# Optimization experiments

Hardware: AMD Instinct MI355X
Metric: run time of the kernel (lower is better)

The kernel has to match this reference:

```python
import jax, jax.numpy as jnp
import numpy as np

N_NODES = 50000
N_EDGES = 800000

def _sage_conv(x, src, dst, W, b, n_nodes):
    # DGL SAGEConv aggregator_type='gcn':
    #   h_neigh = (sum_{u in N(v)} x_u + x_v) / (in_deg(v) + 1)
    #   out = h_neigh @ W.T + b   (fc_self unused for gcn aggregator)
    agg = jax.ops.segment_sum(x[src], dst, num_segments=n_nodes)  # [N, d]
    deg = jax.ops.segment_sum(jnp.ones((src.shape[0],), x.dtype), dst, num_segments=n_nodes)
    h = (agg + x) / (deg + 1.0)[:, None]
    return h @ W.T + b

def setup_inputs() -> dict:
    key = jax.random.key(0)
    ks = jax.random.split(key, 9)
    d_in, d_hid, d_out = 128, 128, 64
    x = jax.random.normal(ks[0], (N_NODES, d_in), dtype=jnp.float32)
    src = jax.random.randint(ks[1], (N_EDGES,), 0, N_NODES, dtype=jnp.int32)
    dst = jax.random.randint(ks[2], (N_EDGES,), 0, N_NODES, dtype=jnp.int32)
    def glorot(k, shape):
        fan = shape[0] + shape[1]
        return jax.random.normal(k, shape, dtype=jnp.float32) * jnp.sqrt(2.0 / fan)
    W1 = glorot(ks[3], (d_hid, d_in))
    b1 = jnp.zeros((d_hid,), jnp.float32)
    W2 = glorot(ks[4], (d_hid, d_hid))
    b2 = jnp.zeros((d_hid,), jnp.float32)
    W3 = glorot(ks[5], (d_out, d_hid))
    b3 = jnp.zeros((d_out,), jnp.float32)
    return {"x": x, "src": src, "dst": dst, "W1": W1, "b1": b1,
            "W2": W2, "b2": b2, "W3": W3, "b3": b3}

def reference(x, src, dst, W1, b1, W2, b2, W3, b3):
    n = x.shape[0]
    h = jax.nn.relu(_sage_conv(x, src, dst, W1, b1, n))
    h = jax.nn.relu(_sage_conv(h, src, dst, W2, b2, n))
    h = jax.nn.sigmoid(_sage_conv(h, src, dst, W3, b3, n))
    return h
```

## Files before the change

kernel.cpp:

```cpp
#include <hip/hip_runtime.h>
#include <hip/hip_bf16.h>
#include <math.h>


#define NFEAT 128
#define BSH   7
#define NBUKP 512
#define EPB2  1024
#define CAP   4000

typedef __attribute__((ext_vector_type(8))) short bf16x8;
typedef __attribute__((ext_vector_type(4))) float f32x4;

__device__ __forceinline__ unsigned short f2bf(float f) {
    unsigned u = __float_as_uint(f);
    u += 0x7fffu + ((u >> 16) & 1u);
    return (unsigned short)(u >> 16);
}
__device__ __forceinline__ float bflo(unsigned u) { return __uint_as_float(u << 16); }
__device__ __forceinline__ float bfhi(unsigned u) { return __uint_as_float(u & 0xffff0000u); }


__global__ __launch_bounds__(256) void build_scatter(const int* __restrict__ src,
                                                     const int* __restrict__ dst,
                                                     int* __restrict__ cursor,
                                                     unsigned long long* __restrict__ pairs,
                                                     int E) {
    __shared__ int hist[NBUKP];
    __shared__ int sc[NBUKP];
    __shared__ int lcur[NBUKP];
    __shared__ int lbase[NBUKP];
    __shared__ unsigned long long stage[EPB2];
    __shared__ int destIdx[EPB2];
    __shared__ int nLocalSh;

    const int t = threadIdx.x;
    hist[t] = 0; hist[t + 256] = 0;
    lcur[t] = 0; lcur[t + 256] = 0;
    __syncthreads();

    const int base = blockIdx.x * EPB2;
    int bb[EPB2 / 256];
    unsigned long long pr[EPB2 / 256];
#pragma unroll
    for (int j = 0; j < EPB2 / 256; ++j) {
        int e = base + t + 256 * j;
        bb[j] = -1;
        if (e < E) {
            int s = src[e], d = dst[e];
            int b = d >> BSH;
            bb[j] = b;
            pr[j] = ((unsigned long long)(unsigned)d << 32) | (unsigned)s;
            atomicAdd(&hist[b], 1);
        }
    }
    __syncthreads();
    sc[t] = hist[t]; sc[t + 256] = hist[t + 256];
    __syncthreads();
    for (int off = 1; off < NBUKP; off <<= 1) {
        int v0 = (t >= off) ? sc[t - off] : 0;
        int v1 = (t + 256 >= off) ? sc[t + 256 - off] : 0;
        __syncthreads();
        sc[t] += v0; sc[t + 256] += v1;
        __syncthreads();
    }
    if (t == 255) nLocalSh = sc[NBUKP - 1];
    sc[t] -= hist[t]; sc[t + 256] -= hist[t + 256];
    for (int b = t; b < NBUKP; b += 256) {
        int h = hist[b];
        if (h > 0) lbase[b] = atomicAdd(&cursor[b], h);
    }
    __syncthreads();
#pragma unroll
    for (int j = 0; j < EPB2 / 256; ++j) {
        int b = bb[j];
        if (b >= 0) {
            int slot = atomicAdd(&lcur[b], 1);
            int spos = sc[b] + slot;
            stage[spos] = pr[j];
            int rel = lbase[b] + slot;
            destIdx[spos] = (rel < CAP) ? (b * CAP + rel) : -1;
        }
    }
    __syncthreads();
    const int nLocal = nLocalSh;
#pragma unroll
    for (int j = 0; j < EPB2 / 256; ++j) {
        int i = t + 256 * j;
        if (i < nLocal && destIdx[i] >= 0) pairs[destIdx[i]] = stage[i];
    }
}


__global__ __launch_bounds__(256) void build_csr(const unsigned long long* __restrict__ pairs,
                                                 const int* __restrict__ cursor,
                                                 int* __restrict__ row_beg,
                                                 int* __restrict__ row_end,
                                                 float* __restrict__ deg_inv,
                                                 int* __restrict__ col_idx, int N) {
    __shared__ unsigned long long pairsL[CAP];
    __shared__ int srcS[CAP];
    __shared__ int nhist[128];
    __shared__ int npref[128];
    __shared__ int ncur[128];

    const int t = threadIdx.x;
    const int b = blockIdx.x;
    const int nodeBase = b << BSH;
    const int eBeg = b * CAP;
    int eCnt = cursor[b];
    if (eCnt > CAP) eCnt = CAP;

    if (t < 128) { nhist[t] = 0; ncur[t] = 0; }
    __syncthreads();

    for (int i = t; i < eCnt; i += 256) {
        unsigned long long p = pairs[eBeg + i];
        pairsL[i] = p;
        atomicAdd(&nhist[(int)(p >> 32) - nodeBase], 1);
    }
    __syncthreads();
    if (t < 128) npref[t] = nhist[t];
    __syncthreads();
    for (int off = 1; off < 128; off <<= 1) {
        int v = (t < 128 && t >= off) ? npref[t - off] : 0;
        __syncthreads();
        if (t < 128) npref[t] += v;
        __syncthreads();
    }
    if (t < 128) npref[t] -= nhist[t];
    if (t < 128 && nodeBase + t < N) {
        row_beg[nodeBase + t] = eBeg + npref[t];
        row_end[nodeBase + t] = eBeg + npref[t] + nhist[t];
        deg_inv[nodeBase + t] = 1.0f / (float)(nhist[t] + 1);
    }
    __syncthreads();
    for (int i = t; i < eCnt; i += 256) {
        unsigned long long p = pairsL[i];
        int d = (int)(p >> 32) - nodeBase;
        int slot = atomicAdd(&ncur[d], 1);
        srcS[npref[d] + slot] = (int)(unsigned)p;
    }
    __syncthreads();
    for (int i = t; i < eCnt; i += 256) col_idx[eBeg + i] = srcS[i];
}


__global__ __launch_bounds__(256) void cvt_all_kernel(const float* __restrict__ x,
                                                      const float* __restrict__ W1,
                                                      const float* __restrict__ W2,
                                                      const float* __restrict__ W3,
                                                      ushort* __restrict__ xb,
                                                      ushort* __restrict__ w1,
                                                      ushort* __restrict__ w2,
                                                      ushort* __restrict__ w3,
                                                      ushort* __restrict__ h1,
                                                      int* __restrict__ cursor, int nbuk, int N,
                                                      int nx, int n1, int n2, int n3) {
    int i = blockIdx.x * blockDim.x + threadIdx.x;
    if (i < nbuk) cursor[i] = 0;
    if (i < 16) {
        ((uint4*)(xb + (size_t)N * NFEAT))[i] = make_uint4(0, 0, 0, 0);
        ((uint4*)(h1 + (size_t)N * NFEAT))[i] = make_uint4(0, 0, 0, 0);
    }
    const float* src; ushort* dst; int off;
    if (i < nx)                      { src = x;  dst = xb; off = i; }
    else if (i < nx + n1)            { src = W1; dst = w1; off = i - nx; }
    else if (i < nx + n1 + n2)       { src = W2; dst = w2; off = i - nx - n1; }
    else if (i < nx + n1 + n2 + n3)  { src = W3; dst = w3; off = i - nx - n1 - n2; }
    else return;
    float4 f = *(const float4*)(src + (size_t)off * 4);
    *(ushort4*)(dst + (size_t)off * 4) = make_ushort4(f2bf(f.x), f2bf(f.y), f2bf(f.z), f2bf(f.w));
}


#define ACC8(u)                                                     \
    a0 += bflo((u).x); a1 += bfhi((u).x);                           \
    a2 += bflo((u).y); a3 += bfhi((u).y);                           \
    a4 += bflo((u).z); a5 += bfhi((u).z);                           \
    a6 += bflo((u).w); a7 += bfhi((u).w);

template<int SECOND>
__global__ __launch_bounds__(256) void fused_agg_gemm_kernel(
        const ushort* __restrict__ Xb,
        const int* __restrict__ row_beg,
        const int* __restrict__ row_end,
        const float* __restrict__ deg_inv,
        const ushort* __restrict__ Wb,
        const float* __restrict__ bias,
        const ushort* __restrict__ W3b,
        const int* __restrict__ col_idx,
        ushort* __restrict__ outB, int N) {
    __shared__ ushort A[16][136];
    __shared__ ushort H2[SECOND ? 16 : 1][136];

    const int t    = threadIdx.x;
    const int w    = t >> 6;
    const int lane = t & 63;
    const int g    = lane >> 4;
    const int f    = lane & 15;
    const int base = blockIdx.x * 16;
    const uint4* X4 = (const uint4*)Xb;

    {
        const int v = base + w * 4 + g;
        const int beg = (v < N) ? row_beg[v] : 0;
        const int end = (v < N) ? row_end[v] : 0;
        const int deg = end - beg;

        uint4 us = (v < N) ? X4[(size_t)v * 16 + f] : make_uint4(0, 0, 0, 0);
        float inv = (v < N) ? deg_inv[v] : 0.f;

        int c0 = N, c1 = N;
        if (f < deg)      c0 = col_idx[beg + f];
        if (f + 16 < deg) c1 = col_idx[beg + 16 + f];

        int wm = deg;
        wm = max(wm, __shfl_xor(wm, 16, 64));
        wm = max(wm, __shfl_xor(wm, 32, 64));
        const int nf = wm < 32 ? wm : 32;
        const int rounds = (nf + 7) >> 3;

        float a0 = 0.f, a1 = 0.f, a2 = 0.f, a3 = 0.f;
        float a4 = 0.f, a5 = 0.f, a6 = 0.f, a7 = 0.f;

        for (int r = 0; r < rounds; ++r) {
            const int j = r * 8;
            const int cc = (j & 16) ? c1 : c0;
            int s0 = __shfl(cc, (j & 15) + 0, 16);
            int s1 = __shfl(cc, (j & 15) + 1, 16);
            int s2 = __shfl(cc, (j & 15) + 2, 16);
            int s3 = __shfl(cc, (j & 15) + 3, 16);
            int s4 = __shfl(cc, (j & 15) + 4, 16);
            int s5 = __shfl(cc, (j & 15) + 5, 16);
            int s6 = __shfl(cc, (j & 15) + 6, 16);
            int s7 = __shfl(cc, (j & 15) + 7, 16);
            uint4 u0 = X4[(size_t)s0 * 16 + f];
            uint4 u1 = X4[(size_t)s1 * 16 + f];
            uint4 u2 = X4[(size_t)s2 * 16 + f];
            uint4 u3 = X4[(size_t)s3 * 16 + f];
            uint4 u4 = X4[(size_t)s4 * 16 + f];
            uint4 u5 = X4[(size_t)s5 * 16 + f];
            uint4 u6 = X4[(size_t)s6 * 16 + f];
            uint4 u7 = X4[(size_t)s7 * 16 + f];
            ACC8(u0); ACC8(u1); ACC8(u2); ACC8(u3);
            ACC8(u4); ACC8(u5); ACC8(u6); ACC8(u7);
        }
        for (int e = beg + 32; e < end; ++e) {
            uint4 u = X4[(size_t)col_idx[e] * 16 + f];
            ACC8(u);
        }

        if (v < N) {
            uint4 r;
            r.x = (unsigned)f2bf((a0 + bflo(us.x)) * inv) | ((unsigned)f2bf((a1 + bfhi(us.x)) * inv) << 16);
            r.y = (unsigned)f2bf((a2 + bflo(us.y)) * inv) | ((unsigned)f2bf((a3 + bfhi(us.y)) * inv) << 16);
            r.z = (unsigned)f2bf((a4 + bflo(us.z)) * inv) | ((unsigned)f2bf((a5 + bfhi(us.z)) * inv) << 16);
            r.w = (unsigned)f2bf((a6 + bflo(us.w)) * inv) | ((unsigned)f2bf((a7 + bfhi(us.w)) * inv) << 16);
            ((uint4*)&A[w * 4 + g][0])[f] = r;
        }
    }
    __syncthreads();

    const int m    = lane & 15;
    const int quad = lane >> 4;
    f32x4 acc0 = {0.f, 0.f, 0.f, 0.f};
    f32x4 acc1 = {0.f, 0.f, 0.f, 0.f};
    {
        const ushort* arow = &A[m][quad * 8];
        const ushort* wrow = Wb + (size_t)(w * 32 + m) * NFEAT + quad * 8;
#pragma unroll
        for (int k0 = 0; k0 < NFEAT; k0 += 32) {
            bf16x8 a  = *(const bf16x8*)(arow + k0);
            bf16x8 bA = *(const bf16x8*)(wrow + k0);
            bf16x8 bB = *(const bf16x8*)(wrow + 16 * NFEAT + k0);
            acc0 = __builtin_amdgcn_mfma_f32_16x16x32_bf16(a, bA, acc0, 0, 0, 0);
            acc1 = __builtin_amdgcn_mfma_f32_16x16x32_bf16(a, bB, acc1, 0, 0, 0);
        }
    }
    const float bv0 = bias[w * 32 + m];
    const float bv1 = bias[w * 32 + 16 + m];

    if (!SECOND) {
#pragma unroll
        for (int r = 0; r < 4; ++r) {
            int row = base + quad * 4 + r;
            if (row < N) {
                outB[(size_t)row * NFEAT + w * 32 + m]      = f2bf(fmaxf(acc0[r] + bv0, 0.f));
                outB[(size_t)row * NFEAT + w * 32 + 16 + m] = f2bf(fmaxf(acc1[r] + bv1, 0.f));
            }
        }
    } else {
#pragma unroll
        for (int r = 0; r < 4; ++r) {
            H2[quad * 4 + r][w * 32 + m]      = f2bf(fmaxf(acc0[r] + bv0, 0.f));
            H2[quad * 4 + r][w * 32 + 16 + m] = f2bf(fmaxf(acc1[r] + bv1, 0.f));
        }
        __syncthreads();
        f32x4 acc3 = {0.f, 0.f, 0.f, 0.f};
        const ushort* hrow  = &H2[m][quad * 8];
        const ushort* w3row = W3b + (size_t)(w * 16 + m) * NFEAT + quad * 8;
#pragma unroll
        for (int k0 = 0; k0 < NFEAT; k0 += 32) {
            bf16x8 a = *(const bf16x8*)(hrow + k0);
            bf16x8 b = *(const bf16x8*)(w3row + k0);
            acc3 = __builtin_amdgcn_mfma_f32_16x16x32_bf16(a, b, acc3, 0, 0, 0);
        }
#pragma unroll
        for (int r = 0; r < 4; ++r) {
            int row = base + quad * 4 + r;
            if (row < N) outB[(size_t)row * 64 + w * 16 + m] = f2bf(acc3[r]);
        }
    }
}


__global__ __launch_bounds__(256) void agg64_sigmoid_kernel(const ushort* __restrict__ Gb,
                                                            const int* __restrict__ row_beg,
                                                            const int* __restrict__ row_end,
                                                            const float* __restrict__ deg_inv,
                                                            const int* __restrict__ col_idx,
                                                            const float* __restrict__ bias,
                                                            float* __restrict__ out, int N) {
    const int wp   = blockIdx.x * (blockDim.x >> 6) + (threadIdx.x >> 6);
    const int lane = threadIdx.x & 63;
    const int half = lane >> 5;
    const int hl   = lane & 31;
    const int v    = wp * 2 + half;
    const bool act = (v < N);

    int beg = 0, end = 0;
    if (act) { beg = row_beg[v]; end = row_end[v]; }
    const int deg = end - beg;
    const unsigned* Gu = (const unsigned*)Gb;

    int cidx = 2 * N;
    if (hl < deg) cidx = col_idx[beg + hl];

    int wm = max(deg, __shfl_xor(deg, 32, 64));
    const int nfast = wm < 32 ? wm : 32;
    const int rounds = (nfast + 7) >> 3;

    float a0 = 0.f, a1 = 0.f, b0 = 0.f, b1 = 0.f;
    float c0 = 0.f, c1 = 0.f, d0 = 0.f, d1 = 0.f;
    for (int r = 0; r < rounds; ++r) {
        const int j = r * 8;
        int s0 = __shfl(cidx, j + 0, 32);
        int s1 = __shfl(cidx, j + 1, 32);
        int s2 = __shfl(cidx, j + 2, 32);
        int s3 = __shfl(cidx, j + 3, 32);
        int s4 = __shfl(cidx, j + 4, 32);
        int s5 = __shfl(cidx, j + 5, 32);
        int s6 = __shfl(cidx, j + 6, 32);
        int s7 = __shfl(cidx, j + 7, 32);
        unsigned u0 = Gu[(size_t)s0 * 32 + hl];
        unsigned u1 = Gu[(size_t)s1 * 32 + hl];
        unsigned u2 = Gu[(size_t)s2 * 32 + hl];
        unsigned u3 = Gu[(size_t)s3 * 32 + hl];
        unsigned u4 = Gu[(size_t)s4 * 32 + hl];
        unsigned u5 = Gu[(size_t)s5 * 32 + hl];
        unsigned u6 = Gu[(size_t)s6 * 32 + hl];
        unsigned u7 = Gu[(size_t)s7 * 32 + hl];
        a0 += bflo(u0); a1 += bfhi(u0);
        b0 += bflo(u1); b1 += bfhi(u1);
        c0 += bflo(u2); c1 += bfhi(u2);
        d0 += bflo(u3); d1 += bfhi(u3);
        a0 += bflo(u4); a1 += bfhi(u4);
        b0 += bflo(u5); b1 += bfhi(u5);
        c0 += bflo(u6); c1 += bfhi(u6);
        d0 += bflo(u7); d1 += bfhi(u7);
    }
    for (int e = beg + 32; e < end; ++e) {
        unsigned u0 = Gu[(size_t)col_idx[e] * 32 + hl];
        a0 += bflo(u0); a1 += bfhi(u0);
    }
    if (act) {
        unsigned us = Gu[(size_t)v * 32 + hl];
        float inv = deg_inv[v];
        float r0 = (a0 + b0 + c0 + d0 + bflo(us)) * inv + bias[hl * 2 + 0];
        float r1 = (a1 + b1 + c1 + d1 + bfhi(us)) * inv + bias[hl * 2 + 1];
        r0 = 1.0f / (1.0f + __expf(-r0));
        r1 = 1.0f / (1.0f + __expf(-r1));
        *(float2*)(out + (size_t)v * 64 + hl * 2) = make_float2(r0, r1);
    }
}


static inline size_t align256(size_t x) { return (x + 255) & ~(size_t)255; }

extern "C" void kernel_launch(void* const* d_in, const int* in_sizes, int n_in,
                              void* d_out, int out_size, void* d_ws, size_t ws_size,
                              hipStream_t stream) {
    const float* x   = (const float*)d_in[0];
    const int*   src = (const int*)d_in[1];
    const int*   dst = (const int*)d_in[2];
    const float* W1  = (const float*)d_in[3];
    const float* b1  = (const float*)d_in[4];
    const float* W2  = (const float*)d_in[5];
    const float* b2  = (const float*)d_in[6];
    const float* W3  = (const float*)d_in[7];
    const float* b3  = (const float*)d_in[8];
    float*       out = (float*)d_out;

    const int N = in_sizes[0] / NFEAT;
    const int E = in_sizes[1];
    const int D_OUT = in_sizes[7] / NFEAT;
    const int NBUK = (N + (1 << BSH) - 1) >> BSH;
    const int SBLK = (E + EPB2 - 1) / EPB2;

    char* ws = (char*)d_ws;
    int* row_beg      = (int*)ws;  ws += align256((size_t)N * 4);
    int* row_end      = (int*)ws;  ws += align256((size_t)N * 4);
    float* deg_inv    = (float*)ws; ws += align256((size_t)N * 4);
    int* cursor       = (int*)ws;  ws += align256((size_t)NBUKP * 4);
    int* col_idx      = (int*)ws;  ws += align256((size_t)NBUK * CAP * 4);
    ushort* w1bf      = (ushort*)ws; ws += align256((size_t)NFEAT * NFEAT * 2);
    ushort* w2bf      = (ushort*)ws; ws += align256((size_t)NFEAT * NFEAT * 2);
    ushort* w3bf      = (ushort*)ws; ws += align256((size_t)D_OUT * NFEAT * 2);
    ushort* xbf       = (ushort*)ws; ws += align256((size_t)(N + 1) * NFEAT * 2);
    ushort* h1bf      = (ushort*)ws; ws += align256((size_t)(N + 1) * NFEAT * 2);
    ushort* gbf = xbf;
    unsigned long long* pairs = (unsigned long long*)h1bf;

    const int nx = N * NFEAT / 4;
    const int n1 = NFEAT * NFEAT / 4, n2 = NFEAT * NFEAT / 4, n3 = D_OUT * NFEAT / 4;
    cvt_all_kernel<<<(nx + n1 + n2 + n3 + 255) / 256, 256, 0, stream>>>(
        x, W1, W2, W3, xbf, w1bf, w2bf, w3bf, h1bf, cursor, NBUKP, N, nx, n1, n2, n3);

    build_scatter<<<SBLK, 256, 0, stream>>>(src, dst, cursor, pairs, E);
    build_csr<<<NBUK, 256, 0, stream>>>(pairs, cursor, row_beg, row_end, deg_inv, col_idx, N);

    const int fusedBlocks = (N + 15) / 16;
    const int agg64Blocks = (N + 7) / 8;

    fused_agg_gemm_kernel<0><<<fusedBlocks, 256, 0, stream>>>(
        xbf, row_beg, row_end, deg_inv, w1bf, b1, nullptr, col_idx, h1bf, N);
    fused_agg_gemm_kernel<1><<<fusedBlocks, 256, 0, stream>>>(
        h1bf, row_beg, row_end, deg_inv, w2bf, b2, w3bf, col_idx, gbf, N);
    agg64_sigmoid_kernel<<<agg64Blocks, 256, 0, stream>>>(
        gbf, row_beg, row_end, deg_inv, col_idx, b3, out, N);
}
```

Measured before the change: 215.2 us.

## Process 32 nodes per block with two nodes per lane group in fused agg-GEMM

Each 16-lane group now aggregates two destination nodes at once, keeping 16 gathered rows in flight per round instead of 8. The block covers 32 rows, so the weight rows loaded for the MFMA GEMM are reused across two 16-row tiles and the grid is halved. This aims to raise memory-level parallelism in the gather and amortize weight loads. The cost is higher register pressure, which may lower occupancy, and the round count now follows the larger degree of the two nodes.

```diff
diff --git a/kernel.cpp b/kernel.cpp
--- a/kernel.cpp
+++ b/kernel.cpp
@@ -174,11 +174,11 @@
 }
 
 
-#define ACC8(u)                                                     \
-    a0 += bflo((u).x); a1 += bfhi((u).x);                           \
-    a2 += bflo((u).y); a3 += bfhi((u).y);                           \
-    a4 += bflo((u).z); a5 += bfhi((u).z);                           \
-    a6 += bflo((u).w); a7 += bfhi((u).w);
+#define ACC8P(p, u)                                                       \
+    p##0 += bflo((u).x); p##1 += bfhi((u).x);                             \
+    p##2 += bflo((u).y); p##3 += bfhi((u).y);                             \
+    p##4 += bflo((u).z); p##5 += bfhi((u).z);                             \
+    p##6 += bflo((u).w); p##7 += bfhi((u).w);
 
 template<int SECOND>
 __global__ __launch_bounds__(256) void fused_agg_gemm_kernel(
@@ -191,31 +191,39 @@
         const ushort* __restrict__ W3b,
         const int* __restrict__ col_idx,
         ushort* __restrict__ outB, int N) {
-    __shared__ ushort A[16][136];
-    __shared__ ushort H2[SECOND ? 16 : 1][136];
+    __shared__ ushort A[32][136];
+    __shared__ ushort H2[SECOND ? 32 : 1][136];
 
     const int t    = threadIdx.x;
     const int w    = t >> 6;
     const int lane = t & 63;
     const int g    = lane >> 4;
     const int f    = lane & 15;
-    const int base = blockIdx.x * 16;
+    const int base = blockIdx.x * 32;
     const uint4* X4 = (const uint4*)Xb;
 
     {
-        const int v = base + w * 4 + g;
-        const int beg = (v < N) ? row_beg[v] : 0;
-        const int end = (v < N) ? row_end[v] : 0;
-        const int deg = end - beg;
-
-        uint4 us = (v < N) ? X4[(size_t)v * 16 + f] : make_uint4(0, 0, 0, 0);
-        float inv = (v < N) ? deg_inv[v] : 0.f;
-
-        int c0 = N, c1 = N;
-        if (f < deg)      c0 = col_idx[beg + f];
-        if (f + 16 < deg) c1 = col_idx[beg + 16 + f];
-
-        int wm = deg;
+        const int vA = base + w * 8 + g * 2;
+        const int vB = vA + 1;
+        const int begA = (vA < N) ? row_beg[vA] : 0;
+        const int endA = (vA < N) ? row_end[vA] : 0;
+        const int degA = endA - begA;
+        const int begB = (vB < N) ? row_beg[vB] : 0;
+        const int endB = (vB < N) ? row_end[vB] : 0;
+        const int degB = endB - begB;
+
+        uint4 usA = (vA < N) ? X4[(size_t)vA * 16 + f] : make_uint4(0, 0, 0, 0);
+        uint4 usB = (vB < N) ? X4[(size_t)vB * 16 + f] : make_uint4(0, 0, 0, 0);
+        float invA = (vA < N) ? deg_inv[vA] : 0.f;
+        float invB = (vB < N) ? deg_inv[vB] : 0.f;
+
+        int c0A = N, c1A = N, c0B = N, c1B = N;
+        if (f < degA)      c0A = col_idx[begA + f];
+        if (f + 16 < degA) c1A = col_idx[begA + 16 + f];
+        if (f < degB)      c0B = col_idx[begB + f];
+        if (f + 16 < degB) c1B = col_idx[begB + 16 + f];
+
+        int wm = max(degA, degB);
         wm = max(wm, __shfl_xor(wm, 16, 64));
         wm = max(wm, __shfl_xor(wm, 32, 64));
         const int nf = wm < 32 ? wm : 32;
@@ -223,93 +231,135 @@
 
         float a0 = 0.f, a1 = 0.f, a2 = 0.f, a3 = 0.f;
         float a4 = 0.f, a5 = 0.f, a6 = 0.f, a7 = 0.f;
+        float b0 = 0.f, b1 = 0.f, b2 = 0.f, b3 = 0.f;
+        float b4 = 0.f, b5 = 0.f, b6 = 0.f, b7 = 0.f;
 
         for (int r = 0; r < rounds; ++r) {
             const int j = r * 8;
-            const int cc = (j & 16) ? c1 : c0;
-            int s0 = __shfl(cc, (j & 15) + 0, 16);
-            int s1 = __shfl(cc, (j & 15) + 1, 16);
-            int s2 = __shfl(cc, (j & 15) + 2, 16);
-            int s3 = __shfl(cc, (j & 15) + 3, 16);
-            int s4 = __shfl(cc, (j & 15) + 4, 16);
-            int s5 = __shfl(cc, (j & 15) + 5, 16);
-            int s6 = __shfl(cc, (j & 15) + 6, 16);
-            int s7 = __shfl(cc, (j & 15) + 7, 16);
-            uint4 u0 = X4[(size_t)s0 * 16 + f];
-            uint4 u1 = X4[(size_t)s1 * 16 + f];
-            uint4 u2 = X4[(size_t)s2 * 16 + f];
-            uint4 u3 = X4[(size_t)s3 * 16 + f];
-            uint4 u4 = X4[(size_t)s4 * 16 + f];
-            uint4 u5 = X4[(size_t)s5 * 16 + f];
-            uint4 u6 = X4[(size_t)s6 * 16 + f];
-            uint4 u7 = X4[(size_t)s7 * 16 + f];
-            ACC8(u0); ACC8(u1); ACC8(u2); ACC8(u3);
-            ACC8(u4); ACC8(u5); ACC8(u6); ACC8(u7);
-        }
-        for (int e = beg + 32; e < end; ++e) {
+            const int ccA = (j & 16) ? c1A : c0A;
+            const int ccB = (j & 16) ? c1B : c0B;
+            int sA0 = __shfl(ccA, (j & 15) + 0, 16);
+            int sA1 = __shfl(ccA, (j & 15) + 1, 16);
+            int sA2 = __shfl(ccA, (j & 15) + 2, 16);
+            int sA3 = __shfl(ccA, (j & 15) + 3, 16);
+            int sA4 = __shfl(ccA, (j & 15) + 4, 16);
+            int sA5 = __shfl(ccA, (j & 15) + 5, 16);
+            int sA6 = __shfl(ccA, (j & 15) + 6, 16);
+            int sA7 = __shfl(ccA, (j & 15) + 7, 16);
+            int sB0 = __shfl(ccB, (j & 15) + 0, 16);
+            int sB1 = __shfl(ccB, (j & 15) + 1, 16);
+            int sB2 = __shfl(ccB, (j & 15) + 2, 16);
+            int sB3 = __shfl(ccB, (j & 15) + 3, 16);
+            int sB4 = __shfl(ccB, (j & 15) + 4, 16);
+            int sB5 = __shfl(ccB, (j & 15) + 5, 16);
+            int sB6 = __shfl(ccB, (j & 15) + 6, 16);
+            int sB7 = __shfl(ccB, (j & 15) + 7, 16);
+            uint4 uA0 = X4[(size_t)sA0 * 16 + f];
+            uint4 uA1 = X4[(size_t)sA1 * 16 + f];
+            uint4 uA2 = X4[(size_t)sA2 * 16 + f];
+            uint4 uA3 = X4[(size_t)sA3 * 16 + f];
+            uint4 uA4 = X4[(size_t)sA4 * 16 + f];
+            uint4 uA5 = X4[(size_t)sA5 * 16 + f];
+            uint4 uA6 = X4[(size_t)sA6 * 16 + f];
+            uint4 uA7 = X4[(size_t)sA7 * 16 + f];
+            uint4 uB0 = X4[(size_t)sB0 * 16 + f];
+            uint4 uB1 = X4[(size_t)sB1 * 16 + f];
+            uint4 uB2 = X4[(size_t)sB2 * 16 + f];
+            uint4 uB3 = X4[(size_t)sB3 * 16 + f];
+            uint4 uB4 = X4[(size_t)sB4 * 16 + f];
+            uint4 uB5 = X4[(size_t)sB5 * 16 + f];
+            uint4 uB6 = X4[(size_t)sB6 * 16 + f];
+            uint4 uB7 = X4[(size_t)sB7 * 16 + f];
+            ACC8P(a, uA0); ACC8P(a, uA1); ACC8P(a, uA2); ACC8P(a, uA3);
+            ACC8P(a, uA4); ACC8P(a, uA5); ACC8P(a, uA6); ACC8P(a, uA7);
+            ACC8P(b, uB0); ACC8P(b, uB1); ACC8P(b, uB2); ACC8P(b, uB3);
+            ACC8P(b, uB4); ACC8P(b, uB5); ACC8P(b, uB6); ACC8P(b, uB7);
+        }
+        for (int e = begA + 32; e < endA; ++e) {
             uint4 u = X4[(size_t)col_idx[e] * 16 + f];
-            ACC8(u);
-        }
-
-        if (v < N) {
+            ACC8P(a, u);
+        }
+        for (int e = begB + 32; e < endB; ++e) {
+            uint4 u = X4[(size_t)col_idx[e] * 16 + f];
+            ACC8P(b, u);
+        }
+
+        if (vA < N) {
             uint4 r;
-            r.x = (unsigned)f2bf((a0 + bflo(us.x)) * inv) | ((unsigned)f2bf((a1 + bfhi(us.x)) * inv) << 16);
-            r.y = (unsigned)f2bf((a2 + bflo(us.y)) * inv) | ((unsigned)f2bf((a3 + bfhi(us.y)) * inv) << 16);
-            r.z = (unsigned)f2bf((a4 + bflo(us.z)) * inv) | ((unsigned)f2bf((a5 + bfhi(us.z)) * inv) << 16);
-            r.w = (unsigned)f2bf((a6 + bflo(us.w)) * inv) | ((unsigned)f2bf((a7 + bfhi(us.w)) * inv) << 16);
-            ((uint4*)&A[w * 4 + g][0])[f] = r;
+            r.x = (unsigned)f2bf((a0 + bflo(usA.x)) * invA) | ((unsigned)f2bf((a1 + bfhi(usA.x)) * invA) << 16);
+            r.y = (unsigned)f2bf((a2 + bflo(usA.y)) * invA) | ((unsigned)f2bf((a3 + bfhi(usA.y)) * invA) << 16);
+            r.z = (unsigned)f2bf((a4 + bflo(usA.z)) * invA) | ((unsigned)f2bf((a5 + bfhi(usA.z)) * invA) << 16);
+            r.w = (unsigned)f2bf((a6 + bflo(usA.w)) * invA) | ((unsigned)f2bf((a7 + bfhi(usA.w)) * invA) << 16);
+            ((uint4*)&A[w * 8 + g * 2][0])[f] = r;
+        }
+        if (vB < N) {
+            uint4 r;
+            r.x = (unsigned)f2bf((b0 + bflo(usB.x)) * invB) | ((unsigned)f2bf((b1 + bfhi(usB.x)) * invB) << 16);
+            r.y = (unsigned)f2bf((b2 + bflo(usB.y)) * invB) | ((unsigned)f2bf((b3 + bfhi(usB.y)) * invB) << 16);
+            r.z = (unsigned)f2bf((b4 + bflo(usB.z)) * invB) | ((unsigned)f2bf((b5 + bfhi(usB.z)) * invB) << 16);
+            r.w = (unsigned)f2bf((b6 + bflo(usB.w)) * invB) | ((unsigned)f2bf((b7 + bfhi(usB.w)) * invB) << 16);
+            ((uint4*)&A[w * 8 + g * 2 + 1][0])[f] = r;
         }
     }
     __syncthreads();
 
     const int m    = lane & 15;
     const int quad = lane >> 4;
-    f32x4 acc0 = {0.f, 0.f, 0.f, 0.f};
-    f32x4 acc1 = {0.f, 0.f, 0.f, 0.f};
-    {
-        const ushort* arow = &A[m][quad * 8];
-        const ushort* wrow = Wb + (size_t)(w * 32 + m) * NFEAT + quad * 8;
-#pragma unroll
-        for (int k0 = 0; k0 < NFEAT; k0 += 32) {
-            bf16x8 a  = *(const bf16x8*)(arow + k0);
-            bf16x8 bA = *(const bf16x8*)(wrow + k0);
-            bf16x8 bB = *(const bf16x8*)(wrow + 16 * NFEAT + k0);
-            acc0 = __builtin_amdgcn_mfma_f32_16x16x32_bf16(a, bA, acc0, 0, 0, 0);
-            acc1 = __builtin_amdgcn_mfma_f32_16x16x32_bf16(a, bB, acc1, 0, 0, 0);
-        }
-    }
     const float bv0 = bias[w * 32 + m];
     const float bv1 = bias[w * 32 + 16 + m];
 
-    if (!SECOND) {
-#pragma unroll
-        for (int r = 0; r < 4; ++r) {
-            int row = base + quad * 4 + r;
-            if (row < N) {
-                outB[(size_t)row * NFEAT + w * 32 + m]      = f2bf(fmaxf(acc0[r] + bv0, 0.f));
-                outB[(size_t)row * NFEAT + w * 32 + 16 + m] = f2bf(fmaxf(acc1[r] + bv1, 0.f));
+#pragma unroll
+    for (int tile = 0; tile < 2; ++tile) {
+        f32x4 acc0 = {0.f, 0.f, 0.f, 0.f};
+        f32x4 acc1 = {0.f, 0.f, 0.f, 0.f};
+        {
+            const ushort* arow = &A[tile * 16 + m][quad * 8];
+            const ushort* wrow = Wb + (size_t)(w * 32 + m) * NFEAT + quad * 8;
+#pragma unroll
+            for (int k0 = 0; k0 < NFEAT; k0 += 32) {
+                bf16x8 a  = *(const bf16x8*)(arow + k0);
+                bf16x8 bA = *(const bf16x8*)(wrow + k0);
+                bf16x8 bB = *(const bf16x8*)(wrow + 16 * NFEAT + k0);
+                acc0 = __builtin_amdgcn_mfma_f32_16x16x32_bf16(a, bA, acc0, 0, 0, 0);
+                acc1 = __builtin_amdgcn_mfma_f32_16x16x32_bf16(a, bB, acc1, 0, 0, 0);
             }
         }
-    } else {
-#pragma unroll
-        for (int r = 0; r < 4; ++r) {
-            H2[quad * 4 + r][w * 32 + m]      = f2bf(fmaxf(acc0[r] + bv0, 0.f));
-            H2[quad * 4 + r][w * 32 + 16 + m] = f2bf(fmaxf(acc1[r] + bv1, 0.f));
-        }
+        if (!SECOND) {
+#pragma unroll
+            for (int r = 0; r < 4; ++r) {
+                int row = base + tile * 16 + quad * 4 + r;
+                if (row < N) {
+                    outB[(size_t)row * NFEAT + w * 32 + m]      = f2bf(fmaxf(acc0[r] + bv0, 0.f));
+                    outB[(size_t)row * NFEAT + w * 32 + 16 + m] = f2bf(fmaxf(acc1[r] + bv1, 0.f));
+                }
+            }
+        } else {
+#pragma unroll
+            for (int r = 0; r < 4; ++r) {
+                H2[tile * 16 + quad * 4 + r][w * 32 + m]      = f2bf(fmaxf(acc0[r] + bv0, 0.f));
+                H2[tile * 16 + quad * 4 + r][w * 32 + 16 + m] = f2bf(fmaxf(acc1[r] + bv1, 0.f));
+            }
+        }
+    }
+
+    if (SECOND) {
         __syncthreads();
-        f32x4 acc3 = {0.f, 0.f, 0.f, 0.f};
-        const ushort* hrow  = &H2[m][quad * 8];
-        const ushort* w3row = W3b + (size_t)(w * 16 + m) * NFEAT + quad * 8;
-#pragma unroll
-        for (int k0 = 0; k0 < NFEAT; k0 += 32) {
-            bf16x8 a = *(const bf16x8*)(hrow + k0);
-            bf16x8 b = *(const bf16x8*)(w3row + k0);
-            acc3 = __builtin_amdgcn_mfma_f32_16x16x32_bf16(a, b, acc3, 0, 0, 0);
-        }
-#pragma unroll
-        for (int r = 0; r < 4; ++r) {
-            int row = base + quad * 4 + r;
-            if (row < N) outB[(size_t)row * 64 + w * 16 + m] = f2bf(acc3[r]);
+#pragma unroll
+        for (int tile = 0; tile < 2; ++tile) {
+            f32x4 acc3 = {0.f, 0.f, 0.f, 0.f};
+            const ushort* hrow  = &H2[tile * 16 + m][quad * 8];
+            const ushort* w3row = W3b + (size_t)(w * 16 + m) * NFEAT + quad * 8;
+#pragma unroll
+            for (int k0 = 0; k0 < NFEAT; k0 += 32) {
+                bf16x8 a = *(const bf16x8*)(hrow + k0);
+                bf16x8 b = *(const bf16x8*)(w3row + k0);
+                acc3 = __builtin_amdgcn_mfma_f32_16x16x32_bf16(a, b, acc3, 0, 0, 0);
+            }
+#pragma unroll
+            for (int r = 0; r < 4; ++r) {
+                int row = base + tile * 16 + quad * 4 + r;
+                if (row < N) outB[(size_t)row * 64 + w * 16 + m] = f2bf(acc3[r]);
+            }
         }
     }
 }
@@ -430,7 +480,7 @@
     build_scatter<<<SBLK, 256, 0, stream>>>(src, dst, cursor, pairs, E);
     build_csr<<<NBUK, 256, 0, stream>>>(pairs, cursor, row_beg, row_end, deg_inv, col_idx, N);
 
-    const int fusedBlocks = (N + 15) / 16;
+    const int fusedBlocks = (N + 31) / 32;
     const int agg64Blocks = (N + 7) / 8;
 
     fused_agg_gemm_kernel<0><<<fusedBlocks, 256, 0, stream>>>(
```

After: 212.6 us. No clear change (-1.2%).
